# Kernel optimization log

Measured on AMD Instinct MI355X. Metric: run time of the kernel, lower is better.

Reference implementation:

```python
import jax, jax.numpy as jnp
import numpy as np

KH = KW = 3
K = KH * KW
STRIDE = 1
PAD = 1
DIL = 1
DG = 1  # deformable groups


def conv2d(x, w, b):
    out = jax.lax.conv_general_dilated(
        x, w, window_strides=(STRIDE, STRIDE),
        padding=[(PAD, PAD), (PAD, PAD)], rhs_dilation=(DIL, DIL),
        dimension_numbers=('NCHW', 'OIHW', 'NCHW'))
    return out + b[None, :, None, None]


def deform_conv2d(x, offset, mask, w, b):
    """DCNv2: bilinear sample at predicted offsets, modulate by mask, GEMM with w."""
    B, Cin, H, W = x.shape
    Ho, Wo = offset.shape[2], offset.shape[3]
    cpg = Cin // DG
    # torchvision layout: channel 2*(g*K+k) = dy, 2*(g*K+k)+1 = dx
    off = offset.reshape(B, DG, K, 2, Ho, Wo)
    off_y, off_x = off[:, :, :, 0], off[:, :, :, 1]  # [B,DG,K,Ho,Wo]
    m = mask.reshape(B, DG, K, Ho, Wo)
    ky = jnp.repeat(jnp.arange(KH), KW) * DIL          # [K] kernel row offsets
    kx = jnp.tile(jnp.arange(KW), KH) * DIL            # [K] kernel col offsets
    hh = jnp.arange(Ho) * STRIDE - PAD
    ww = jnp.arange(Wo) * STRIDE - PAD
    py = off_y + ky[None, None, :, None, None] + hh[None, None, None, :, None]
    px = off_x + kx[None, None, :, None, None] + ww[None, None, None, None, :]
    y0 = jnp.floor(py); x0 = jnp.floor(px)
    wy = py - y0; wx = px - x0
    x_g = x.reshape(B, DG, cpg, H * W)

    def gather(yc, xc):  # zero-padded bilinear corner fetch
        valid = ((yc >= 0) & (yc < H) & (xc >= 0) & (xc < W)).astype(x.dtype)
        yi = jnp.clip(yc, 0, H - 1).astype(jnp.int32)
        xi = jnp.clip(xc, 0, W - 1).astype(jnp.int32)
        idx = (yi * W + xi).reshape(B, DG, 1, K * Ho * Wo)
        v = jnp.take_along_axis(x_g, jnp.broadcast_to(idx, (B, DG, cpg, K * Ho * Wo)), axis=3)
        return v.reshape(B, DG, cpg, K, Ho, Wo) * valid[:, :, None]

    v00 = gather(y0, x0)
    v01 = gather(y0, x0 + 1)
    v10 = gather(y0 + 1, x0)
    v11 = gather(y0 + 1, x0 + 1)
    wy_b = wy[:, :, None]; wx_b = wx[:, :, None]  # broadcast over cpg
    sampled = (v00 * (1 - wy_b) * (1 - wx_b) + v01 * (1 - wy_b) * wx_b
               + v10 * wy_b * (1 - wx_b) + v11 * wy_b * wx_b)
    sampled = (sampled * m[:, :, None]).reshape(B, Cin, K, Ho, Wo)
    Cout = w.shape[0]
    out = jnp.einsum('bckhw,ock->bohw', sampled, w.reshape(Cout, Cin, K))
    return out + b[None, :, None, None]


def setup_inputs() -> dict:
    key = jax.random.key(0)
    k1, k2, k3, k4 = jax.random.split(key, 4)
    B, Cin, Cout, H, W = 8, 128, 128, 64, 64
    omc = DG * 3 * K  # 2*K offsets + K mask channels = 27
    x = jax.random.normal(k1, (B, Cin, H, W), dtype=jnp.float32)
    # small offset-conv weights -> modest predicted offsets (mimics near-zero init)
    w_off = jax.random.normal(k2, (omc, Cin, KH, KW), dtype=jnp.float32) * 0.01
    b_off = jnp.zeros((omc,), dtype=jnp.float32)
    w_def = jax.random.normal(k3, (Cout, Cin, KH, KW), dtype=jnp.float32) * (1.0 / np.sqrt(Cin * K))
    b_def = jax.random.normal(k4, (Cout,), dtype=jnp.float32) * 0.01
    return {"x": x, "w_off": w_off, "b_off": b_off, "w_def": w_def, "b_def": b_def}


def reference(x, w_off, b_off, w_def, b_def):
    out = conv2d(x, w_off, b_off)
    oc = DG * 2 * K
    offset = out[:, :oc]
    mask = jax.nn.sigmoid(out[:, oc:])
    return deform_conv2d(x, offset, mask, w_def, b_def)
```

## Files before the change

### kernel.cpp

```cpp
#include <hip/hip_runtime.h>
#include <math.h>

typedef _Float16 f16;
typedef __attribute__((ext_vector_type(2))) _Float16 f16x2;
typedef __attribute__((ext_vector_type(8))) _Float16 f16x8;
typedef __attribute__((ext_vector_type(4))) float f32x4;

#define NBATCH 8
#define WSA_ELE 36864
#define WSB_ELE 147456
#define OFF_WSB  73728
#define OFF_XT   368640
#define OFF_OFFM 8757248

__device__ __forceinline__ void gload_lds16(const f16* gsrc, f16* ldst) {
  __builtin_amdgcn_global_load_lds(
      (const __attribute__((address_space(1))) unsigned int*)gsrc,
      (__attribute__((address_space(3))) unsigned int*)ldst, 16, 0, 0);
}

__global__ __launch_bounds__(256) void prep_w_kernel(const float* __restrict__ w_off,
                                                     const float* __restrict__ w_def,
                                                     f16* __restrict__ wsA,
                                                     f16* __restrict__ wsB) {
  int i = blockIdx.x * 256 + threadIdx.x;
  if (i < WSA_ELE) {
    int j = i & 7, lane = (i >> 3) & 63, fm = i >> 9;
    int ch = fm >> 1, mt = fm & 1;
    int row = mt * 16 + (lane & 15);
    int kidx = ch * 32 + (lane >> 4) * 8 + j;
    int k = kidx >> 7, cc = kidx & 127;
    float v = (row < 27) ? w_off[row * 1152 + cc * 9 + k] : 0.0f;
    wsA[i] = (f16)v;
  } else {
    int e = i - WSA_ELE;
    int j = e & 7, lane = (e >> 3) & 63, fm = e >> 9;
    int ch = fm >> 3, mt = fm & 7;
    int row = mt * 16 + (lane & 15);
    int kidx = ch * 32 + (lane >> 4) * 8 + j;
    int k = kidx >> 7, cc = kidx & 127;
    wsB[e] = (f16)w_def[row * 1152 + cc * 9 + k];
  }
}

__global__ __launch_bounds__(256) void transpose_kernel(const float* __restrict__ x,
                                                        f16* __restrict__ xt) {
  __shared__ f16 s_t[128 * 66];
  const int t = threadIdx.x;
  const int b = blockIdx.x >> 6;
  const int pos0 = (blockIdx.x & 63) << 6;
  const float* xb = x + ((size_t)b << 19);
  for (int i = t; i < 8192; i += 256) {
    int c = i >> 6, p = i & 63;
    s_t[c * 66 + p] = (f16)xb[c * 4096 + pos0 + p];
  }
  __syncthreads();
  f16* xtb = xt + ((size_t)b << 19);
  for (int i = t; i < 4096; i += 256) {
    int p = i >> 6, c2 = (i & 63) * 2;
    unsigned v0 = *(const unsigned short*)&s_t[c2 * 66 + p];
    unsigned v1 = *(const unsigned short*)&s_t[(c2 + 1) * 66 + p];
    *(unsigned*)&xtb[(size_t)(pos0 + p) * 128 + c2] = v0 | (v1 << 16);
  }
}

__global__ __launch_bounds__(256) void offset_conv_kernel(const f16* __restrict__ xt,
                                                          const f16* __restrict__ wsA,
                                                          const float* __restrict__ b_off,
                                                          float* __restrict__ offm) {
  const int t = threadIdx.x;
  const int b = blockIdx.x >> 6, ho = blockIdx.x & 63;
  const int lane = t & 63, wid = t >> 6;
  const int q = lane >> 4, li = lane & 15;
  const int px = (wid << 4) + li;
  const char* xtb = (const char*)xt + ((size_t)b << 20);

  f32x4 acc0 = {0.f, 0.f, 0.f, 0.f}, acc1 = {0.f, 0.f, 0.f, 0.f};

  for (int k = 0; k < 9; ++k) {
    const int ky = k / 3, kx = k - ky * 3;
    const int y = ho + ky - 1;
    const int xx = px + kx - 1;
    const bool valid = ((unsigned)y < 64u) && ((unsigned)xx < 64u);
    const int pos = min(max(y, 0), 63) * 64 + min(max(xx, 0), 63);
    const int voff = pos * 256 + q * 16;
    #pragma unroll
    for (int c4 = 0; c4 < 4; ++c4) {
      union { uint4 u; f16x8 v; } bu;
      bu.u = *(const uint4*)(xtb + voff + c4 * 64);
      if (!valid) { bu.u.x = 0u; bu.u.y = 0u; bu.u.z = 0u; bu.u.w = 0u; }
      const int ch = k * 4 + c4;
      f16x8 a0 = *(const f16x8*)&wsA[(ch * 2    ) * 512 + lane * 8];
      f16x8 a1 = *(const f16x8*)&wsA[(ch * 2 + 1) * 512 + lane * 8];
      acc0 = __builtin_amdgcn_mfma_f32_16x16x32_f16(a0, bu.v, acc0, 0, 0, 0);
      acc1 = __builtin_amdgcn_mfma_f32_16x16x32_f16(a1, bu.v, acc1, 0, 0, 0);
    }
  }

  float* om = offm + (size_t)b * 27 * 4096 + ho * 64 + px;
  #pragma unroll
  for (int mt = 0; mt < 2; ++mt) {
    f32x4 a = mt ? acc1 : acc0;
    #pragma unroll
    for (int r = 0; r < 4; ++r) {
      int oc = mt * 16 + q * 4 + r;
      if (oc < 27) {
        float v = a[r] + b_off[oc];
        if (oc >= 18) v = 1.0f / (1.0f + __expf(-v));
        om[oc * 4096] = v;
      }
    }
  }
}

__global__ __launch_bounds__(256) void dcn_kernel(const f16* __restrict__ xt,
                                                  const f16* __restrict__ wsB,
                                                  const float* __restrict__ offm,
                                                  const float* __restrict__ b_def,
                                                  float* __restrict__ out) {
  __shared__ uint4  s_ofs[576];
  __shared__ float4 s_wt[576];
  __shared__ __align__(16) f16 s_a[2][4096];
  const int t = threadIdx.x;
  const int b = blockIdx.x >> 6, ho = blockIdx.x & 63;
  const int lane = t & 63, wid = t >> 6;
  const int q = lane >> 4, li = lane & 15;
  const int px0 = wid << 4;
  const char* xtb = (const char*)xt + ((size_t)b << 20);

  {
    const int seg = wid * 2;
    gload_lds16(wsB + seg * 512 + lane * 8,       &s_a[0][seg * 512]);
    gload_lds16(wsB + (seg + 1) * 512 + lane * 8, &s_a[0][(seg + 1) * 512]);
  }

  const float* ob = offm + (size_t)b * 27 * 4096 + ho * 64;
  for (int f = t; f < 576; f += 256) {
    int k = f >> 6, p = f & 63;
    int ky = k / 3, kx = k - ky * 3;
    float oy = ob[(2 * k    ) * 4096 + p];
    float ox = ob[(2 * k + 1) * 4096 + p];
    float m  = ob[(18 + k   ) * 4096 + p];
    float py  = oy + (float)(ho + ky - 1);
    float pxf = ox + (float)(p + kx - 1);
    float y0f = floorf(py), x0f = floorf(pxf);
    float wy = py - y0f, wx = pxf - x0f;
    int y0 = (int)y0f, x0 = (int)x0f;
    int y1 = y0 + 1, x1 = x0 + 1;
    bool y0v = (unsigned)y0 < 64u, y1v = (unsigned)y1 < 64u;
    bool x0v = (unsigned)x0 < 64u, x1v = (unsigned)x1 < 64u;
    int y0c = min(max(y0, 0), 63), y1c = min(max(y1, 0), 63);
    int x0c = min(max(x0, 0), 63), x1c = min(max(x1, 0), 63);
    uint4 o4;
    o4.x = (unsigned)((y0c * 64 + x0c) * 256);
    o4.y = (unsigned)((y0c * 64 + x1c) * 256);
    o4.z = (unsigned)((y1c * 64 + x0c) * 256);
    o4.w = (unsigned)((y1c * 64 + x1c) * 256);
    float4 w4;
    w4.x = (y0v && x0v) ? (1.f - wy) * (1.f - wx) * m : 0.f;
    w4.y = (y0v && x1v) ? (1.f - wy) * wx         * m : 0.f;
    w4.z = (y1v && x0v) ? wy         * (1.f - wx) * m : 0.f;
    w4.w = (y1v && x1v) ? wy         * wx         * m : 0.f;
    s_ofs[f] = o4;
    s_wt[f]  = w4;
  }
  __syncthreads();

  f32x4 acc[8];
  #pragma unroll
  for (int mt = 0; mt < 8; ++mt) acc[mt] = (f32x4){0.f, 0.f, 0.f, 0.f};

  for (int k = 0; k < 9; ++k) {
    const int e = k * 64 + px0 + li;
    const uint4  o4 = s_ofs[e];
    const float4 w4 = s_wt[e];
    const unsigned voff0 = o4.x + q * 16, voff1 = o4.y + q * 16;
    const unsigned voff2 = o4.z + q * 16, voff3 = o4.w + q * 16;
    const f16 h0 = (f16)w4.x, h1 = (f16)w4.y, h2 = (f16)w4.z, h3 = (f16)w4.w;
    const f16x2 wp0 = {h0, h0}, wp1 = {h1, h1}, wp2 = {h2, h2}, wp3 = {h3, h3};
    #pragma unroll
    for (int c4 = 0; c4 < 4; ++c4) {
      const int ch = k * 4 + c4;
      if (ch < 35) {
        const int nb = (ch + 1) & 1;
        const int seg = wid * 2;
        const f16* src = wsB + (ch + 1) * 4096;
        gload_lds16(src + seg * 512 + lane * 8,       &s_a[nb][seg * 512]);
        gload_lds16(src + (seg + 1) * 512 + lane * 8, &s_a[nb][(seg + 1) * 512]);
      }
      union { uint4 u; f16x2 h[4]; } d0, d1, d2, d3;
      d0.u = *(const uint4*)(xtb + voff0 + c4 * 64);
      d1.u = *(const uint4*)(xtb + voff1 + c4 * 64);
      d2.u = *(const uint4*)(xtb + voff2 + c4 * 64);
      d3.u = *(const uint4*)(xtb + voff3 + c4 * 64);
      union { f16x2 h[4]; f16x8 v; } bf;
      #pragma unroll
      for (int i = 0; i < 4; ++i) {
        f16x2 s = d0.h[i] * wp0;
        s = s + d1.h[i] * wp1;
        s = s + d2.h[i] * wp2;
        s = s + d3.h[i] * wp3;
        bf.h[i] = s;
      }
      const f16* ab = &s_a[ch & 1][0];
      #pragma unroll
      for (int mt = 0; mt < 8; ++mt) {
        f16x8 a = *(const f16x8*)&ab[(mt * 64 + lane) * 8];
        acc[mt] = __builtin_amdgcn_mfma_f32_16x16x32_f16(a, bf.v, acc[mt], 0, 0, 0);
      }
      __syncthreads();
    }
  }

  float* o = out + (size_t)b * 128 * 4096 + ho * 64 + px0 + li;
  #pragma unroll
  for (int mt = 0; mt < 8; ++mt) {
    #pragma unroll
    for (int r = 0; r < 4; ++r) {
      int oc = mt * 16 + q * 4 + r;
      o[oc * 4096] = acc[mt][r] + b_def[oc];
    }
  }
}

extern "C" void kernel_launch(void* const* d_in, const int* in_sizes, int n_in,
                              void* d_out, int out_size, void* d_ws, size_t ws_size,
                              hipStream_t stream) {
  const float* x     = (const float*)d_in[0];
  const float* w_off = (const float*)d_in[1];
  const float* b_off = (const float*)d_in[2];
  const float* w_def = (const float*)d_in[3];
  const float* b_def = (const float*)d_in[4];
  float* out = (float*)d_out;

  f16*   wsA  = (f16*)d_ws;
  f16*   wsB  = (f16*)((char*)d_ws + OFF_WSB);
  f16*   xt   = (f16*)((char*)d_ws + OFF_XT);
  float* offm = (float*)((char*)d_ws + OFF_OFFM);

  prep_w_kernel<<<dim3((WSA_ELE + WSB_ELE) / 256), dim3(256), 0, stream>>>(w_off, w_def, wsA, wsB);
  transpose_kernel<<<dim3(NBATCH * 64), dim3(256), 0, stream>>>(x, xt);
  offset_conv_kernel<<<dim3(NBATCH * 64), dim3(256), 0, stream>>>(xt, wsA, b_off, offm);
  dcn_kernel<<<dim3(NBATCH * 64), dim3(256), 0, stream>>>(xt, wsB, offm, b_def, out);
}
```

Measured before the change: 135.7 us.

## Merge prep kernels, compact DCN sample tables, and cut per-chunk barriers

```diff
diff --git a/kernel.cpp b/kernel.cpp
--- a/kernel.cpp
+++ b/kernel.cpp
@@ -3,12 +3,14 @@
 
 typedef _Float16 f16;
 typedef __attribute__((ext_vector_type(2))) _Float16 f16x2;
+typedef __attribute__((ext_vector_type(4))) _Float16 f16x4;
 typedef __attribute__((ext_vector_type(8))) _Float16 f16x8;
 typedef __attribute__((ext_vector_type(4))) float f32x4;
 
 #define NBATCH 8
 #define WSA_ELE 36864
 #define WSB_ELE 147456
+#define PREP_BLOCKS 720
 #define OFF_WSB  73728
 #define OFF_XT   368640
 #define OFF_OFFM 8757248
@@ -19,48 +21,51 @@
       (__attribute__((address_space(3))) unsigned int*)ldst, 16, 0, 0);
 }
 
-__global__ __launch_bounds__(256) void prep_w_kernel(const float* __restrict__ w_off,
-                                                     const float* __restrict__ w_def,
-                                                     f16* __restrict__ wsA,
-                                                     f16* __restrict__ wsB) {
-  int i = blockIdx.x * 256 + threadIdx.x;
-  if (i < WSA_ELE) {
-    int j = i & 7, lane = (i >> 3) & 63, fm = i >> 9;
-    int ch = fm >> 1, mt = fm & 1;
-    int row = mt * 16 + (lane & 15);
-    int kidx = ch * 32 + (lane >> 4) * 8 + j;
-    int k = kidx >> 7, cc = kidx & 127;
-    float v = (row < 27) ? w_off[row * 1152 + cc * 9 + k] : 0.0f;
-    wsA[i] = (f16)v;
+__global__ __launch_bounds__(256) void prep_kernel(const float* __restrict__ x,
+                                                   const float* __restrict__ w_off,
+                                                   const float* __restrict__ w_def,
+                                                   f16* __restrict__ wsA,
+                                                   f16* __restrict__ wsB,
+                                                   f16* __restrict__ xt) {
+  __shared__ f16 s_t[128 * 66];
+  const int bid = blockIdx.x;
+  const int t = threadIdx.x;
+  if (bid < PREP_BLOCKS) {
+    int i = bid * 256 + t;
+    if (i < WSA_ELE) {
+      int j = i & 7, lane = (i >> 3) & 63, fm = i >> 9;
+      int ch = fm >> 1, mt = fm & 1;
+      int row = mt * 16 + (lane & 15);
+      int kidx = ch * 32 + (lane >> 4) * 8 + j;
+      int k = kidx >> 7, cc = kidx & 127;
+      float v = (row < 27) ? w_off[row * 1152 + cc * 9 + k] : 0.0f;
+      wsA[i] = (f16)v;
+    } else {
+      int e = i - WSA_ELE;
+      int j = e & 7, lane = (e >> 3) & 63, fm = e >> 9;
+      int ch = fm >> 3, mt = fm & 7;
+      int row = mt * 16 + (lane & 15);
+      int kidx = ch * 32 + (lane >> 4) * 8 + j;
+      int k = kidx >> 7, cc = kidx & 127;
+      wsB[e] = (f16)w_def[row * 1152 + cc * 9 + k];
+    }
   } else {
-    int e = i - WSA_ELE;
-    int j = e & 7, lane = (e >> 3) & 63, fm = e >> 9;
-    int ch = fm >> 3, mt = fm & 7;
-    int row = mt * 16 + (lane & 15);
-    int kidx = ch * 32 + (lane >> 4) * 8 + j;
-    int k = kidx >> 7, cc = kidx & 127;
-    wsB[e] = (f16)w_def[row * 1152 + cc * 9 + k];
-  }
-}
-
-__global__ __launch_bounds__(256) void transpose_kernel(const float* __restrict__ x,
-                                                        f16* __restrict__ xt) {
-  __shared__ f16 s_t[128 * 66];
-  const int t = threadIdx.x;
-  const int b = blockIdx.x >> 6;
-  const int pos0 = (blockIdx.x & 63) << 6;
-  const float* xb = x + ((size_t)b << 19);
-  for (int i = t; i < 8192; i += 256) {
-    int c = i >> 6, p = i & 63;
-    s_t[c * 66 + p] = (f16)xb[c * 4096 + pos0 + p];
-  }
-  __syncthreads();
-  f16* xtb = xt + ((size_t)b << 19);
-  for (int i = t; i < 4096; i += 256) {
-    int p = i >> 6, c2 = (i & 63) * 2;
-    unsigned v0 = *(const unsigned short*)&s_t[c2 * 66 + p];
-    unsigned v1 = *(const unsigned short*)&s_t[(c2 + 1) * 66 + p];
-    *(unsigned*)&xtb[(size_t)(pos0 + p) * 128 + c2] = v0 | (v1 << 16);
+    const int bb = bid - PREP_BLOCKS;
+    const int b = bb >> 6;
+    const int pos0 = (bb & 63) << 6;
+    const float* xb = x + ((size_t)b << 19);
+    for (int i = t; i < 8192; i += 256) {
+      int c = i >> 6, p = i & 63;
+      s_t[c * 66 + p] = (f16)xb[c * 4096 + pos0 + p];
+    }
+    __syncthreads();
+    f16* xtb = xt + ((size_t)b << 19);
+    for (int i = t; i < 4096; i += 256) {
+      int p = i >> 6, c2 = (i & 63) * 2;
+      unsigned v0 = *(const unsigned short*)&s_t[c2 * 66 + p];
+      unsigned v1 = *(const unsigned short*)&s_t[(c2 + 1) * 66 + p];
+      *(unsigned*)&xtb[(size_t)(pos0 + p) * 128 + c2] = v0 | (v1 << 16);
+    }
   }
 }
 
@@ -113,26 +118,20 @@
   }
 }
 
-__global__ __launch_bounds__(256) void dcn_kernel(const f16* __restrict__ xt,
-                                                  const f16* __restrict__ wsB,
-                                                  const float* __restrict__ offm,
-                                                  const float* __restrict__ b_def,
-                                                  float* __restrict__ out) {
-  __shared__ uint4  s_ofs[576];
-  __shared__ float4 s_wt[576];
-  __shared__ __align__(16) f16 s_a[2][4096];
+__global__ __launch_bounds__(256, 5) void dcn_kernel(const f16* __restrict__ xt,
+                                                     const f16* __restrict__ wsB,
+                                                     const float* __restrict__ offm,
+                                                     const float* __restrict__ b_def,
+                                                     float* __restrict__ out) {
+  __shared__ ushort4 s_pos[576];
+  __shared__ f16x4   s_wth[576];
+  __shared__ __align__(16) f16 s_a[8192];
   const int t = threadIdx.x;
   const int b = blockIdx.x >> 6, ho = blockIdx.x & 63;
   const int lane = t & 63, wid = t >> 6;
   const int q = lane >> 4, li = lane & 15;
   const int px0 = wid << 4;
   const char* xtb = (const char*)xt + ((size_t)b << 20);
-
-  {
-    const int seg = wid * 2;
-    gload_lds16(wsB + seg * 512 + lane * 8,       &s_a[0][seg * 512]);
-    gload_lds16(wsB + (seg + 1) * 512 + lane * 8, &s_a[0][(seg + 1) * 512]);
-  }
 
   const float* ob = offm + (size_t)b * 27 * 4096 + ho * 64;
   for (int f = t; f < 576; f += 256) {
@@ -151,64 +150,61 @@
     bool x0v = (unsigned)x0 < 64u, x1v = (unsigned)x1 < 64u;
     int y0c = min(max(y0, 0), 63), y1c = min(max(y1, 0), 63);
     int x0c = min(max(x0, 0), 63), x1c = min(max(x1, 0), 63);
-    uint4 o4;
-    o4.x = (unsigned)((y0c * 64 + x0c) * 256);
-    o4.y = (unsigned)((y0c * 64 + x1c) * 256);
-    o4.z = (unsigned)((y1c * 64 + x0c) * 256);
-    o4.w = (unsigned)((y1c * 64 + x1c) * 256);
-    float4 w4;
-    w4.x = (y0v && x0v) ? (1.f - wy) * (1.f - wx) * m : 0.f;
-    w4.y = (y0v && x1v) ? (1.f - wy) * wx         * m : 0.f;
-    w4.z = (y1v && x0v) ? wy         * (1.f - wx) * m : 0.f;
-    w4.w = (y1v && x1v) ? wy         * wx         * m : 0.f;
-    s_ofs[f] = o4;
-    s_wt[f]  = w4;
-  }
-  __syncthreads();
+    ushort4 p4;
+    p4.x = (unsigned short)(y0c * 64 + x0c);
+    p4.y = (unsigned short)(y0c * 64 + x1c);
+    p4.z = (unsigned short)(y1c * 64 + x0c);
+    p4.w = (unsigned short)(y1c * 64 + x1c);
+    f16x4 wh;
+    wh[0] = (f16)((y0v && x0v) ? (1.f - wy) * (1.f - wx) * m : 0.f);
+    wh[1] = (f16)((y0v && x1v) ? (1.f - wy) * wx         * m : 0.f);
+    wh[2] = (f16)((y1v && x0v) ? wy         * (1.f - wx) * m : 0.f);
+    wh[3] = (f16)((y1v && x1v) ? wy         * wx         * m : 0.f);
+    s_pos[f] = p4;
+    s_wth[f] = wh;
+  }
 
   f32x4 acc[8];
   #pragma unroll
   for (int mt = 0; mt < 8; ++mt) acc[mt] = (f32x4){0.f, 0.f, 0.f, 0.f};
 
-  for (int k = 0; k < 9; ++k) {
+  for (int c4g = 0; c4g < 36; ++c4g) {
+    const int k = c4g >> 2, c4 = c4g & 3, sub = c4g & 1;
+    if (sub == 0) {
+      __syncthreads();
+      const f16* src = wsB + c4g * 4096 + wid * 2048 + lane * 8;
+      f16* dst = &s_a[wid * 2048];
+      gload_lds16(src,        dst);
+      gload_lds16(src +  512, dst +  512);
+      gload_lds16(src + 1024, dst + 1024);
+      gload_lds16(src + 1536, dst + 1536);
+      __syncthreads();
+    }
     const int e = k * 64 + px0 + li;
-    const uint4  o4 = s_ofs[e];
-    const float4 w4 = s_wt[e];
-    const unsigned voff0 = o4.x + q * 16, voff1 = o4.y + q * 16;
-    const unsigned voff2 = o4.z + q * 16, voff3 = o4.w + q * 16;
-    const f16 h0 = (f16)w4.x, h1 = (f16)w4.y, h2 = (f16)w4.z, h3 = (f16)w4.w;
-    const f16x2 wp0 = {h0, h0}, wp1 = {h1, h1}, wp2 = {h2, h2}, wp3 = {h3, h3};
-    #pragma unroll
-    for (int c4 = 0; c4 < 4; ++c4) {
-      const int ch = k * 4 + c4;
-      if (ch < 35) {
-        const int nb = (ch + 1) & 1;
-        const int seg = wid * 2;
-        const f16* src = wsB + (ch + 1) * 4096;
-        gload_lds16(src + seg * 512 + lane * 8,       &s_a[nb][seg * 512]);
-        gload_lds16(src + (seg + 1) * 512 + lane * 8, &s_a[nb][(seg + 1) * 512]);
-      }
-      union { uint4 u; f16x2 h[4]; } d0, d1, d2, d3;
-      d0.u = *(const uint4*)(xtb + voff0 + c4 * 64);
-      d1.u = *(const uint4*)(xtb + voff1 + c4 * 64);
-      d2.u = *(const uint4*)(xtb + voff2 + c4 * 64);
-      d3.u = *(const uint4*)(xtb + voff3 + c4 * 64);
-      union { f16x2 h[4]; f16x8 v; } bf;
-      #pragma unroll
-      for (int i = 0; i < 4; ++i) {
-        f16x2 s = d0.h[i] * wp0;
-        s = s + d1.h[i] * wp1;
-        s = s + d2.h[i] * wp2;
-        s = s + d3.h[i] * wp3;
-        bf.h[i] = s;
-      }
-      const f16* ab = &s_a[ch & 1][0];
-      #pragma unroll
-      for (int mt = 0; mt < 8; ++mt) {
-        f16x8 a = *(const f16x8*)&ab[(mt * 64 + lane) * 8];
-        acc[mt] = __builtin_amdgcn_mfma_f32_16x16x32_f16(a, bf.v, acc[mt], 0, 0, 0);
-      }
-      __syncthreads();
+    const ushort4 p4 = s_pos[e];
+    const f16x4   w4 = s_wth[e];
+    const unsigned cb = (unsigned)(c4 * 64 + q * 16);
+    union { uint4 u; f16x2 h[4]; } d0, d1, d2, d3;
+    d0.u = *(const uint4*)(xtb + (((unsigned)p4.x << 8) + cb));
+    d1.u = *(const uint4*)(xtb + (((unsigned)p4.y << 8) + cb));
+    d2.u = *(const uint4*)(xtb + (((unsigned)p4.z << 8) + cb));
+    d3.u = *(const uint4*)(xtb + (((unsigned)p4.w << 8) + cb));
+    const f16x2 wp0 = {w4[0], w4[0]}, wp1 = {w4[1], w4[1]};
+    const f16x2 wp2 = {w4[2], w4[2]}, wp3 = {w4[3], w4[3]};
+    union { f16x2 h[4]; f16x8 v; } bf;
+    #pragma unroll
+    for (int i = 0; i < 4; ++i) {
+      f16x2 s = d0.h[i] * wp0;
+      s = s + d1.h[i] * wp1;
+      s = s + d2.h[i] * wp2;
+      s = s + d3.h[i] * wp3;
+      bf.h[i] = s;
+    }
+    const f16* ab = &s_a[sub * 4096];
+    #pragma unroll
+    for (int mt = 0; mt < 8; ++mt) {
+      f16x8 a = *(const f16x8*)&ab[(mt * 64 + lane) * 8];
+      acc[mt] = __builtin_amdgcn_mfma_f32_16x16x32_f16(a, bf.v, acc[mt], 0, 0, 0);
     }
   }
 
@@ -238,8 +234,7 @@
   f16*   xt   = (f16*)((char*)d_ws + OFF_XT);
   float* offm = (float*)((char*)d_ws + OFF_OFFM);
 
-  prep_w_kernel<<<dim3((WSA_ELE + WSB_ELE) / 256), dim3(256), 0, stream>>>(w_off, w_def, wsA, wsB);
-  transpose_kernel<<<dim3(NBATCH * 64), dim3(256), 0, stream>>>(x, xt);
+  prep_kernel<<<dim3(PREP_BLOCKS + NBATCH * 64), dim3(256), 0, stream>>>(x, w_off, w_def, wsA, wsB, xt);
   offset_conv_kernel<<<dim3(NBATCH * 64), dim3(256), 0, stream>>>(xt, wsA, b_off, offm);
   dcn_kernel<<<dim3(NBATCH * 64), dim3(256), 0, stream>>>(xt, wsB, offm, b_def, out);
 }
```

Result: no change. 136.0 us (+0.3%).
